# Performance work log

Hardware: AMD Instinct MI355X
Metric: run time of the kernel (lower is better)

## Reference

```python
import jax, jax.numpy as jnp
import numpy as np

B = 8        # number of clouds
NP = 4096    # points per cloud
STRIDE = 4   # sampler stride -> NS = NP // STRIDE sampled centers per cloud
K = 32       # knn neighbours
NS = NP // STRIDE


def setup_inputs() -> dict:
    key = jax.random.key(0)
    k1, k2, k3, k4 = jax.random.split(key, 4)
    N = B * NP
    x = jax.random.normal(k1, (N, 64), dtype=jnp.float32)
    pos = jax.random.normal(k2, (N, 3), dtype=jnp.float32)
    batch = jnp.repeat(jnp.arange(B, dtype=jnp.int64), NP)
    d_in = 64 + 3
    W1 = jax.random.normal(k3, (d_in, 128), dtype=jnp.float32) / np.sqrt(d_in)
    b1 = jnp.zeros((128,), dtype=jnp.float32)
    W2 = jax.random.normal(k4, (128, 256), dtype=jnp.float32) / np.sqrt(128)
    b2 = jnp.zeros((256,), dtype=jnp.float32)
    return {"x": x, "pos": pos, "batch": batch, "W1": W1, "b1": b1, "W2": W2, "b2": b2}


def reference(x, pos, batch, W1, b1, W2, b2):
    # --- sampler: stride sampling per cloud (clouds are equal-sized, contiguous) ---
    pos_b = pos.reshape(B, NP, 3)
    idx_local = jnp.arange(0, NP, STRIDE)                       # [NS]
    idx = (idx_local[None, :] + jnp.arange(B)[:, None] * NP).reshape(-1)  # global sampled idx [B*NS]
    pos_s = pos_b[:, idx_local]                                 # [B, NS, 3]

    # --- neighbour_finder: knn within each cloud (batch-respecting via per-cloud blocks) ---
    # squared distances [B, NS, NP] without materializing [B,NS,NP,3]
    d2 = ((pos_s ** 2).sum(-1)[:, :, None]
          + (pos_b ** 2).sum(-1)[:, None, :]
          - 2.0 * jnp.einsum('bsd,bnd->bsn', pos_s, pos_b))
    _, nbr = jax.lax.top_k(-d2, K)                              # [B, NS, K] local neighbour idx
    col = (nbr + (jnp.arange(B) * NP)[:, None, None]).reshape(-1)  # global neighbour idx [E]

    # --- conv: PointNetConv -> MLP(concat(x_j, pos_j - pos_i)) then max over neighbours ---
    x_j = x[col].reshape(B, NS, K, -1)                          # [B, NS, K, 64]
    rel = pos[col].reshape(B, NS, K, 3) - pos_s[:, :, None, :]  # pos_j - pos_i
    feat = jnp.concatenate([x_j, rel], axis=-1)                 # [B, NS, K, 67]
    h = jax.nn.relu(feat @ W1 + b1)                             # [B, NS, K, 128]
    h = jax.nn.relu(h @ W2 + b2)                                # [B, NS, K, 256]
    x_out = h.max(axis=2).reshape(B * NS, -1)                   # [B*NS, 256]

    pos_out = pos_s.reshape(-1, 3)
    batch_out = batch[idx]
    return x_out, pos_out, batch_out, idx
```

## Files before the change

kernel.cpp:

```cpp
#include <hip/hip_runtime.h>
#include <hip/hip_bf16.h>

#define BB 8
#define NP 4096
#define STRIDE 4
#define KNN 32
#define NS (NP/STRIDE)
#define NQ (BB*NS)
#define DIN 67
#define H1N 128
#define H2N 256

typedef __attribute__((ext_vector_type(8)))  short bf16x8;
typedef __attribute__((ext_vector_type(16))) float f32x16;
typedef __attribute__((ext_vector_type(8)))  short short8;

__device__ __forceinline__ unsigned int f2u(float f) {
    unsigned int b = __float_as_uint(f);
    return (b & 0x80000000u) ? ~b : (b | 0x80000000u);
}
__device__ __forceinline__ short f2bf(float f) {
    unsigned u = __float_as_uint(f);
    unsigned r = u + 0x7FFFu + ((u >> 16) & 1u);
    return (short)(r >> 16);
}

__global__ __launch_bounds__(256) void knn_kernel(const float* __restrict__ pos,
                                                  int* __restrict__ col) {
    __shared__ unsigned long long surv[NP];
    __shared__ unsigned int pvt[4];
    __shared__ int scount;

    const int q    = blockIdx.x;
    const int b    = q >> 10;
    const int s    = q & (NS - 1);
    const int qi   = b * NP + s * STRIDE;
    const int t    = threadIdx.x;
    const int lane = t & 63;

    if (t == 64) pvt[3] = 0xFFFFFFFFu;

    const float qx = pos[qi*3+0], qy = pos[qi*3+1], qz = pos[qi*3+2];
    const float q2 = __fadd_rn(__fadd_rn(__fmul_rn(qx,qx), __fmul_rn(qy,qy)), __fmul_rn(qz,qz));

    const float* pb = pos + (size_t)b * NP * 3;
    unsigned int myk[16];
    #pragma unroll
    for (int i = 0; i < 4; ++i) {
        const int u = t + i * 256;
        const float4* pp = (const float4*)(pb + (size_t)u * 12);
        const float4 v0 = pp[0], v1 = pp[1], v2 = pp[2];
        const float px[4] = {v0.x, v0.w, v1.z, v2.y};
        const float py[4] = {v0.y, v1.x, v1.w, v2.z};
        const float pz[4] = {v0.z, v1.y, v2.x, v2.w};
        #pragma unroll
        for (int j = 0; j < 4; ++j) {
            const float p2 = __fadd_rn(__fadd_rn(__fmul_rn(px[j],px[j]), __fmul_rn(py[j],py[j])), __fmul_rn(pz[j],pz[j]));
            const float dt = __fadd_rn(__fadd_rn(__fmul_rn(qx,px[j]), __fmul_rn(qy,py[j])), __fmul_rn(qz,pz[j]));
            const float d2 = __fsub_rn(__fadd_rn(q2, p2), __fmul_rn(2.0f, dt));
            myk[i*4+j] = f2u(d2);
        }
    }

    if (t < 64) {
        const unsigned int mk = myk[0];
        int rank = 0;
        #pragma unroll
        for (int ss = 0; ss < 64; ++ss) {
            const unsigned int ks = __shfl(mk, ss, 64);
            rank += (int)((ks < mk) | ((ks == mk) & (ss < t)));
        }
        if (rank == 1)  pvt[0] = mk;
        if (rank == 4)  pvt[1] = mk;
        if (rank == 16) pvt[2] = mk;
    }
    __syncthreads();

    int C = 0;
    for (int level = 0; level < 4 && C < KNN; ++level) {
        __syncthreads();
        if (t == 0) scount = 0;
        __syncthreads();
        const unsigned int T = pvt[level];
        #pragma unroll
        for (int i = 0; i < 16; ++i) {
            const bool p = (myk[i] <= T);
            const unsigned long long mask = __ballot(p);
            const int cnt = __popcll(mask);
            int base = 0;
            if (lane == 0 && cnt) base = atomicAdd(&scount, cnt);
            base = __shfl(base, 0, 64);
            if (p) {
                const int off = __popcll(mask & ((1ull << lane) - 1ull));
                const int n   = 4 * (t + (i >> 2) * 256) + (i & 3);
                surv[base + off] = ((unsigned long long)myk[i] << 32) | (unsigned int)n;
            }
        }
        __syncthreads();
        C = scount;
    }

    const int L = C;
    for (int j = t; j < L; j += 256) {
        const unsigned long long v = surv[j];
        int rank = 0;
        #pragma unroll 4
        for (int ss = 0; ss < L; ++ss)
            rank += (int)(surv[ss] < v);
        if (rank < KNN)
            col[q * KNN + rank] = b * NP + (int)(unsigned int)(v & 0xFFFFFFFFull);
    }
}

__global__ __launch_bounds__(64) void prep_w1(const float* __restrict__ W1,
                                              short* __restrict__ W1T) {
    const int nt = blockIdx.x / 5, t = blockIdx.x % 5;
    const int l  = threadIdx.x;
    const int c  = 32*nt + (l & 31);
    short8 v;
    #pragma unroll
    for (int b = 0; b < 8; ++b) {
        const int k = 16*t + 8*(l >> 5) + b;
        v[b] = (k < DIN) ? f2bf(W1[k * H1N + c]) : (short)0;
    }
    *(short8*)(W1T + ((size_t)(nt*5 + t) * 64 + l) * 8) = v;
}

__global__ __launch_bounds__(64) void prep_w2(const float* __restrict__ W2,
                                              short* __restrict__ W2T) {
    const int nt = blockIdx.x >> 3, t = blockIdx.x & 7;
    const int l  = threadIdx.x;
    const int c  = 32*nt + (l & 31);
    short8 v;
    #pragma unroll
    for (int b = 0; b < 8; ++b) {
        const int k = 16*t + 8*(l >> 5) + b;
        v[b] = f2bf(W2[k * H2N + c]);
    }
    *(short8*)(W2T + ((size_t)(nt*8 + t) * 64 + l) * 8) = v;
}

__global__ __launch_bounds__(256, 2) void mlp_mfma(const float* __restrict__ x,
                                                   const float* __restrict__ pos,
                                                   const int* __restrict__ col,
                                                   const float* __restrict__ b1,
                                                   const float* __restrict__ b2,
                                                   const short* __restrict__ W1T,
                                                   const short* __restrict__ W2T,
                                                   float* __restrict__ out) {
    __shared__ __align__(16) short feat[128 * 80];
    __shared__ __align__(16) short h1s [128 * 128];

    const int q0 = blockIdx.x * 4;
    const int t  = threadIdx.x;
    const int w  = t >> 6, l = t & 63;

    {
        const int row  = t >> 1, part = t & 1;
        const int q    = q0 + (row >> 5);
        const int c    = col[q * KNN + (row & 31)];
        const float4* xr = (const float4*)(x + (size_t)c * 64 + part * 32);
        short* fr = feat + row * 80 + part * 32;
        #pragma unroll
        for (int i = 0; i < 8; ++i) {
            const float4 v = xr[i];
            *(int*)(fr + i * 4 + 0) = (int)((unsigned short)f2bf(v.x) | ((unsigned)(unsigned short)f2bf(v.y) << 16));
            *(int*)(fr + i * 4 + 2) = (int)((unsigned short)f2bf(v.z) | ((unsigned)(unsigned short)f2bf(v.w) << 16));
        }
        if (part == 0) {
            const int b  = q >> 10;
            const int qi = b * NP + (q & (NS - 1)) * STRIDE;
            short8 o;
            o[0] = f2bf(pos[c*3+0] - pos[qi*3+0]);
            o[1] = f2bf(pos[c*3+1] - pos[qi*3+1]);
            o[2] = f2bf(pos[c*3+2] - pos[qi*3+2]);
            o[3] = 0; o[4] = 0; o[5] = 0; o[6] = 0; o[7] = 0;
            *(short8*)(feat + row * 80 + 64) = o;
            short8 z = {0,0,0,0,0,0,0,0};
            *(short8*)(feat + row * 80 + 72) = z;
        }
    }
    __syncthreads();

    const int lr = l & 31;
    const int lh = l >> 5;

    {
        bf16x8 w1f[20];
        #pragma unroll
        for (int i = 0; i < 20; ++i)
            w1f[i] = *(const bf16x8*)(W1T + ((size_t)i * 64 + l) * 8);

        bf16x8 a1[5];
        #pragma unroll
        for (int kt = 0; kt < 5; ++kt) {
            const int row = 32*w + lr;
            a1[kt] = *(const bf16x8*)(feat + row * 80 + 16*kt + 8*lh);
        }

        #pragma unroll
        for (int nt = 0; nt < 4; ++nt) {
            const float bv = b1[32*nt + lr];
            f32x16 acc;
            #pragma unroll
            for (int r = 0; r < 16; ++r) acc[r] = bv;
            #pragma unroll
            for (int kt = 0; kt < 5; ++kt)
                acc = __builtin_amdgcn_mfma_f32_32x32x16_bf16(a1[kt], w1f[nt*5 + kt], acc, 0, 0, 0);
            #pragma unroll
            for (int r = 0; r < 16; ++r) {
                const int i   = (r & 3) + 8*(r >> 2) + 4*lh;
                const int row = 32*w + i;
                const int c   = 32*nt + lr;
                const int adr = row * 128 + ((((c >> 3) ^ (row & 15)) << 3) | (c & 7));
                h1s[adr] = f2bf(fmaxf(acc[r], 0.0f));
            }
        }
    }
    __syncthreads();

    {
        bf16x8 a2[8];
        #pragma unroll
        for (int kt = 0; kt < 8; ++kt) {
            const int row  = 32*w + lr;
            const int slot = 2*kt + lh;
            a2[kt] = *(const bf16x8*)(h1s + row * 128 + ((slot ^ (row & 15)) << 3));
        }

        f32x16 acc[8];
        #pragma unroll
        for (int nt = 0; nt < 8; ++nt)
            #pragma unroll
            for (int r = 0; r < 16; ++r) acc[nt][r] = 0.0f;

        bf16x8 cur[8];
        #pragma unroll
        for (int kt = 0; kt < 8; ++kt)
            cur[kt] = *(const bf16x8*)(W2T + ((size_t)kt * 64 + l) * 8);

        #pragma unroll
        for (int nt = 0; nt < 8; ++nt) {
            bf16x8 nxt[8];
            if (nt < 7) {
                #pragma unroll
                for (int kt = 0; kt < 8; ++kt)
                    nxt[kt] = *(const bf16x8*)(W2T + ((size_t)((nt+1)*8 + kt) * 64 + l) * 8);
            }
            #pragma unroll
            for (int kt = 0; kt < 8; ++kt)
                acc[nt] = __builtin_amdgcn_mfma_f32_32x32x16_bf16(a2[kt], cur[kt], acc[nt], 0, 0, 0);
            #pragma unroll
            for (int kt = 0; kt < 8; ++kt) cur[kt] = nxt[kt];
        }

        const int q = q0 + w;
        #pragma unroll
        for (int nt = 0; nt < 8; ++nt) {
            float m = acc[nt][0];
            #pragma unroll
            for (int r = 1; r < 16; ++r) m = fmaxf(m, acc[nt][r]);
            m = fmaxf(m, __shfl_xor(m, 32, 64));
            m = fmaxf(m + b2[32*nt + lr], 0.0f);
            if (l < 32) out[(size_t)q * H2N + 32*nt + l] = m;
        }
    }
}

__global__ __launch_bounds__(256) void tail_kernel(const float* __restrict__ pos,
                                                   float* __restrict__ out) {
    const int qn = blockIdx.x * 256 + threadIdx.x;
    if (qn >= NQ) return;
    const int b  = qn >> 10;
    const int s  = qn & (NS - 1);
    const int qi = b * NP + s * STRIDE;

    float* pos_out   = out + (size_t)NQ * H2N;
    float* batch_out = pos_out + (size_t)NQ * 3;
    float* idx_out   = batch_out + NQ;

    pos_out[qn*3+0] = pos[qi*3+0];
    pos_out[qn*3+1] = pos[qi*3+1];
    pos_out[qn*3+2] = pos[qi*3+2];
    batch_out[qn]   = (float)b;
    idx_out[qn]     = (float)qi;
}

extern "C" void kernel_launch(void* const* d_in, const int* in_sizes, int n_in,
                              void* d_out, int out_size, void* d_ws, size_t ws_size,
                              hipStream_t stream) {
    const float* x   = (const float*)d_in[0];
    const float* pos = (const float*)d_in[1];
    const float* W1  = (const float*)d_in[3];
    const float* b1  = (const float*)d_in[4];
    const float* W2  = (const float*)d_in[5];
    const float* b2  = (const float*)d_in[6];
    float* out = (float*)d_out;

    char* ws   = (char*)d_ws;
    int*  col  = (int*)ws;
    short* W1T = (short*)(ws + 1048576);
    short* W2T = (short*)(ws + 1048576 + 20480);

    prep_w1<<<20, 64, 0, stream>>>(W1, W1T);
    prep_w2<<<64, 64, 0, stream>>>(W2, W2T);
    knn_kernel<<<NQ, 256, 0, stream>>>(pos, col);
    mlp_mfma<<<NQ/4, 256, 0, stream>>>(x, pos, col, b1, b2, W1T, W2T, out);
    tail_kernel<<<(NQ + 255) / 256, 256, 0, stream>>>(pos, out);
}
```

Measured before the change: 156.0 us.

## Count survivors per threshold before compaction and vectorize rank scan

The KNN selection now counts survivors per wave with ballots for each threshold level and compacts only once, at the first level that yields at least K candidates. Per-ballot atomics on a shared counter are replaced by deterministic per-wave prefix offsets. The pivot ranks are lowered (1/3/8 instead of 1/4/16), giving tighter thresholds and a smaller survivor set. The final rank scan reads pairs of 64-bit keys per shared-memory load. Tighter pivots may fall through to wider levels more often, which costs extra count passes.

```diff
diff --git a/kernel.cpp b/kernel.cpp
--- a/kernel.cpp
+++ b/kernel.cpp
@@ -27,15 +27,16 @@
 
 __global__ __launch_bounds__(256) void knn_kernel(const float* __restrict__ pos,
                                                   int* __restrict__ col) {
-    __shared__ unsigned long long surv[NP];
+    __shared__ __align__(16) unsigned long long surv[NP];
     __shared__ unsigned int pvt[4];
-    __shared__ int scount;
+    __shared__ int cnts[4];
 
     const int q    = blockIdx.x;
     const int b    = q >> 10;
     const int s    = q & (NS - 1);
     const int qi   = b * NP + s * STRIDE;
     const int t    = threadIdx.x;
+    const int w    = t >> 6;
     const int lane = t & 63;
 
     if (t == 64) pvt[3] = 0xFFFFFFFFu;
@@ -70,43 +71,56 @@
             const unsigned int ks = __shfl(mk, ss, 64);
             rank += (int)((ks < mk) | ((ks == mk) & (ss < t)));
         }
-        if (rank == 1)  pvt[0] = mk;
-        if (rank == 4)  pvt[1] = mk;
-        if (rank == 16) pvt[2] = mk;
+        if (rank == 1) pvt[0] = mk;
+        if (rank == 3) pvt[1] = mk;
+        if (rank == 8) pvt[2] = mk;
     }
     __syncthreads();
 
-    int C = 0;
-    for (int level = 0; level < 4 && C < KNN; ++level) {
+    int C = 0, level = 0;
+    for (; level < 4; ++level) {
+        const unsigned int T = pvt[level];
+        int cw = 0;
+        #pragma unroll
+        for (int i = 0; i < 16; ++i)
+            cw += __popcll(__ballot(myk[i] <= T));
+        if (lane == 0) cnts[w] = cw;
         __syncthreads();
-        if (t == 0) scount = 0;
+        C = cnts[0] + cnts[1] + cnts[2] + cnts[3];
+        if (C >= KNN) break;
         __syncthreads();
+    }
+
+    {
         const unsigned int T = pvt[level];
+        int base = 0;
+        #pragma unroll
+        for (int i = 0; i < 4; ++i) base += (i < w) ? cnts[i] : 0;
         #pragma unroll
         for (int i = 0; i < 16; ++i) {
             const bool p = (myk[i] <= T);
             const unsigned long long mask = __ballot(p);
-            const int cnt = __popcll(mask);
-            int base = 0;
-            if (lane == 0 && cnt) base = atomicAdd(&scount, cnt);
-            base = __shfl(base, 0, 64);
             if (p) {
                 const int off = __popcll(mask & ((1ull << lane) - 1ull));
                 const int n   = 4 * (t + (i >> 2) * 256) + (i & 3);
                 surv[base + off] = ((unsigned long long)myk[i] << 32) | (unsigned int)n;
             }
-        }
-        __syncthreads();
-        C = scount;
-    }
-
-    const int L = C;
-    for (int j = t; j < L; j += 256) {
+            base += __popcll(mask);
+        }
+    }
+    __syncthreads();
+
+    const ulonglong2* sp2 = (const ulonglong2*)surv;
+    const int C2 = C >> 1;
+    for (int j = t; j < C; j += 256) {
         const unsigned long long v = surv[j];
         int rank = 0;
         #pragma unroll 4
-        for (int ss = 0; ss < L; ++ss)
-            rank += (int)(surv[ss] < v);
+        for (int ss = 0; ss < C2; ++ss) {
+            const ulonglong2 pr = sp2[ss];
+            rank += (int)(pr.x < v) + (int)(pr.y < v);
+        }
+        if (C & 1) rank += (int)(surv[C - 1] < v);
         if (rank < KNN)
             col[q * KNN + rank] = b * NP + (int)(unsigned int)(v & 0xFFFFFFFFull);
     }
```

Measured after the change: 160.2 us. +2.7%, slower.

## Run kNN one query per wavefront and fuse tail and weight-prep kernels

Applied to the files above, without the earlier changes.

The kNN kernel now gives each query one wavefront instead of a full 256-thread block. Distances are recomputed during each threshold compaction pass, and pivots are chosen from a 64-point strided sample with an adaptive threshold retry loop. This removes the block-level barriers, the shared atomics and the register-held keys. The tail outputs are folded into the kNN kernel and the two weight-prep kernels are merged into one, which cuts launch count. In exchange, distances may be recomputed several times per query, and survivors are capped at 1024 per wave. Hitting that cap could truncate candidates.

```diff
diff --git a/kernel.cpp b/kernel.cpp
--- a/kernel.cpp
+++ b/kernel.cpp
@@ -10,6 +10,7 @@
 #define DIN 67
 #define H1N 128
 #define H2N 256
+#define SCAPW 1024
 
 typedef __attribute__((ext_vector_type(8)))  short bf16x8;
 typedef __attribute__((ext_vector_type(16))) float f32x16;
@@ -26,118 +27,139 @@
 }
 
 __global__ __launch_bounds__(256) void knn_kernel(const float* __restrict__ pos,
-                                                  int* __restrict__ col) {
-    __shared__ unsigned long long surv[NP];
-    __shared__ unsigned int pvt[4];
-    __shared__ int scount;
-
-    const int q    = blockIdx.x;
+                                                  int* __restrict__ col,
+                                                  float* __restrict__ out) {
+    __shared__ __align__(16) unsigned long long surv[4][SCAPW];
+
+    const int t    = threadIdx.x;
+    const int w    = t >> 6;
+    const int lane = t & 63;
+    const int q    = blockIdx.x * 4 + w;
     const int b    = q >> 10;
     const int s    = q & (NS - 1);
     const int qi   = b * NP + s * STRIDE;
-    const int t    = threadIdx.x;
-    const int lane = t & 63;
-
-    if (t == 64) pvt[3] = 0xFFFFFFFFu;
 
     const float qx = pos[qi*3+0], qy = pos[qi*3+1], qz = pos[qi*3+2];
     const float q2 = __fadd_rn(__fadd_rn(__fmul_rn(qx,qx), __fmul_rn(qy,qy)), __fmul_rn(qz,qz));
-
     const float* pb = pos + (size_t)b * NP * 3;
-    unsigned int myk[16];
+
+    {
+        float* pos_out   = out + (size_t)NQ * H2N;
+        float* batch_out = pos_out + (size_t)NQ * 3;
+        float* idx_out   = batch_out + NQ;
+        if (lane < 3)       pos_out[q*3+lane] = pos[qi*3+lane];
+        else if (lane == 3) batch_out[q] = (float)b;
+        else if (lane == 4) idx_out[q]   = (float)qi;
+    }
+
+    unsigned int skey;
+    {
+        const int n = lane * 64;
+        const float px = pb[n*3+0], py = pb[n*3+1], pz = pb[n*3+2];
+        const float p2 = __fadd_rn(__fadd_rn(__fmul_rn(px,px), __fmul_rn(py,py)), __fmul_rn(pz,pz));
+        const float dt = __fadd_rn(__fadd_rn(__fmul_rn(qx,px), __fmul_rn(qy,py)), __fmul_rn(qz,pz));
+        skey = f2u(__fsub_rn(__fadd_rn(q2, p2), __fmul_rn(2.0f, dt)));
+    }
+    int srk = 0;
     #pragma unroll
-    for (int i = 0; i < 4; ++i) {
-        const int u = t + i * 256;
-        const float4* pp = (const float4*)(pb + (size_t)u * 12);
-        const float4 v0 = pp[0], v1 = pp[1], v2 = pp[2];
-        const float px[4] = {v0.x, v0.w, v1.z, v2.y};
-        const float py[4] = {v0.y, v1.x, v1.w, v2.z};
-        const float pz[4] = {v0.z, v1.y, v2.x, v2.w};
-        #pragma unroll
-        for (int j = 0; j < 4; ++j) {
-            const float p2 = __fadd_rn(__fadd_rn(__fmul_rn(px[j],px[j]), __fmul_rn(py[j],py[j])), __fmul_rn(pz[j],pz[j]));
-            const float dt = __fadd_rn(__fadd_rn(__fmul_rn(qx,px[j]), __fmul_rn(qy,py[j])), __fmul_rn(qz,pz[j]));
-            const float d2 = __fsub_rn(__fadd_rn(q2, p2), __fmul_rn(2.0f, dt));
-            myk[i*4+j] = f2u(d2);
-        }
-    }
-
-    if (t < 64) {
-        const unsigned int mk = myk[0];
-        int rank = 0;
-        #pragma unroll
-        for (int ss = 0; ss < 64; ++ss) {
-            const unsigned int ks = __shfl(mk, ss, 64);
-            rank += (int)((ks < mk) | ((ks == mk) & (ss < t)));
-        }
-        if (rank == 1)  pvt[0] = mk;
-        if (rank == 4)  pvt[1] = mk;
-        if (rank == 16) pvt[2] = mk;
-    }
-    __syncthreads();
-
-    int C = 0;
-    for (int level = 0; level < 4 && C < KNN; ++level) {
-        __syncthreads();
-        if (t == 0) scount = 0;
-        __syncthreads();
-        const unsigned int T = pvt[level];
-        #pragma unroll
-        for (int i = 0; i < 16; ++i) {
-            const bool p = (myk[i] <= T);
-            const unsigned long long mask = __ballot(p);
-            const int cnt = __popcll(mask);
-            int base = 0;
-            if (lane == 0 && cnt) base = atomicAdd(&scount, cnt);
-            base = __shfl(base, 0, 64);
-            if (p) {
-                const int off = __popcll(mask & ((1ull << lane) - 1ull));
-                const int n   = 4 * (t + (i >> 2) * 256) + (i & 3);
-                surv[base + off] = ((unsigned long long)myk[i] << 32) | (unsigned int)n;
+    for (int ss = 0; ss < 64; ++ss) {
+        const unsigned int ks = (unsigned int)__shfl((int)skey, ss, 64);
+        srk += (int)((ks < skey) | ((ks == skey) & (ss < lane)));
+    }
+    unsigned int T0, T1, T2, T3, T4;
+    {
+        unsigned long long m;
+        m = __ballot(srk == 0);  T0 = (unsigned int)__shfl((int)skey, (int)__builtin_ctzll(m), 64);
+        m = __ballot(srk == 1);  T1 = (unsigned int)__shfl((int)skey, (int)__builtin_ctzll(m), 64);
+        m = __ballot(srk == 3);  T2 = (unsigned int)__shfl((int)skey, (int)__builtin_ctzll(m), 64);
+        m = __ballot(srk == 8);  T3 = (unsigned int)__shfl((int)skey, (int)__builtin_ctzll(m), 64);
+        m = __ballot(srk == 31); T4 = (unsigned int)__shfl((int)skey, (int)__builtin_ctzll(m), 64);
+    }
+
+    unsigned long long* sw = surv[w];
+
+    auto compact = [&](unsigned int T) -> int {
+        int base = 0;
+        #pragma unroll 4
+        for (int j4 = 0; j4 < 16; ++j4) {
+            const int n0 = j4 * 256 + lane * 4;
+            const float4* pp = (const float4*)(pb + (size_t)n0 * 3);
+            const float4 v0 = pp[0], v1 = pp[1], v2 = pp[2];
+            const float px[4] = {v0.x, v0.w, v1.z, v2.y};
+            const float py[4] = {v0.y, v1.x, v1.w, v2.z};
+            const float pz[4] = {v0.z, v1.y, v2.x, v2.w};
+            #pragma unroll
+            for (int jj = 0; jj < 4; ++jj) {
+                const float p2 = __fadd_rn(__fadd_rn(__fmul_rn(px[jj],px[jj]), __fmul_rn(py[jj],py[jj])), __fmul_rn(pz[jj],pz[jj]));
+                const float dt = __fadd_rn(__fadd_rn(__fmul_rn(qx,px[jj]), __fmul_rn(qy,py[jj])), __fmul_rn(qz,pz[jj]));
+                const unsigned int k = f2u(__fsub_rn(__fadd_rn(q2, p2), __fmul_rn(2.0f, dt)));
+                const bool psel = (k <= T);
+                const unsigned long long mask = __ballot(psel);
+                if (psel) {
+                    const int idx = base + (int)__popcll(mask & ((1ull << lane) - 1ull));
+                    if (idx < SCAPW)
+                        sw[idx] = ((unsigned long long)k << 32) | (unsigned int)(n0 + jj);
+                }
+                base += (int)__popcll(mask);
             }
         }
-        __syncthreads();
-        C = scount;
-    }
-
-    const int L = C;
-    for (int j = t; j < L; j += 256) {
-        const unsigned long long v = surv[j];
-        int rank = 0;
+        return base;
+    };
+
+    int lvl = 1, C = 0;
+    #pragma unroll 1
+    for (int att = 0; att < 4; ++att) {
+        const unsigned int T = (lvl == 0) ? T0 : (lvl == 1) ? T1 : (lvl == 2) ? T2 : (lvl == 3) ? T3 : T4;
+        C = compact(T);
+        if (C >= KNN && C <= SCAPW) break;
+        if (C < KNN) { if (lvl >= 4) break; ++lvl; }
+        else         { if (lvl == 0) break; lvl = 0; }
+    }
+    if (C > SCAPW) C = SCAPW;
+
+    const ulonglong2* sp2 = (const ulonglong2*)sw;
+    const int C2 = C >> 1;
+    for (int j = lane; j < C; j += 64) {
+        const unsigned long long v = sw[j];
+        int rk = 0;
         #pragma unroll 4
-        for (int ss = 0; ss < L; ++ss)
-            rank += (int)(surv[ss] < v);
-        if (rank < KNN)
-            col[q * KNN + rank] = b * NP + (int)(unsigned int)(v & 0xFFFFFFFFull);
-    }
-}
-
-__global__ __launch_bounds__(64) void prep_w1(const float* __restrict__ W1,
-                                              short* __restrict__ W1T) {
-    const int nt = blockIdx.x / 5, t = blockIdx.x % 5;
-    const int l  = threadIdx.x;
-    const int c  = 32*nt + (l & 31);
-    short8 v;
-    #pragma unroll
-    for (int b = 0; b < 8; ++b) {
-        const int k = 16*t + 8*(l >> 5) + b;
-        v[b] = (k < DIN) ? f2bf(W1[k * H1N + c]) : (short)0;
-    }
-    *(short8*)(W1T + ((size_t)(nt*5 + t) * 64 + l) * 8) = v;
-}
-
-__global__ __launch_bounds__(64) void prep_w2(const float* __restrict__ W2,
-                                              short* __restrict__ W2T) {
-    const int nt = blockIdx.x >> 3, t = blockIdx.x & 7;
-    const int l  = threadIdx.x;
-    const int c  = 32*nt + (l & 31);
-    short8 v;
-    #pragma unroll
-    for (int b = 0; b < 8; ++b) {
-        const int k = 16*t + 8*(l >> 5) + b;
-        v[b] = f2bf(W2[k * H2N + c]);
-    }
-    *(short8*)(W2T + ((size_t)(nt*8 + t) * 64 + l) * 8) = v;
+        for (int ss = 0; ss < C2; ++ss) {
+            const ulonglong2 pr = sp2[ss];
+            rk += (int)(pr.x < v) + (int)(pr.y < v);
+        }
+        if (C & 1) rk += (int)(sw[C - 1] < v);
+        if (rk < KNN)
+            col[q * KNN + rk] = b * NP + (int)(unsigned int)(v & 0xFFFFFFFFull);
+    }
+}
+
+__global__ __launch_bounds__(64) void prep_w(const float* __restrict__ W1,
+                                             const float* __restrict__ W2,
+                                             short* __restrict__ W1T,
+                                             short* __restrict__ W2T) {
+    const int l = threadIdx.x;
+    if (blockIdx.x < 20) {
+        const int nt = blockIdx.x / 5, t = blockIdx.x % 5;
+        const int c  = 32*nt + (l & 31);
+        short8 v;
+        #pragma unroll
+        for (int b = 0; b < 8; ++b) {
+            const int k = 16*t + 8*(l >> 5) + b;
+            v[b] = (k < DIN) ? f2bf(W1[k * H1N + c]) : (short)0;
+        }
+        *(short8*)(W1T + ((size_t)(nt*5 + t) * 64 + l) * 8) = v;
+    } else {
+        const int bb = blockIdx.x - 20;
+        const int nt = bb >> 3, t = bb & 7;
+        const int c  = 32*nt + (l & 31);
+        short8 v;
+        #pragma unroll
+        for (int b = 0; b < 8; ++b) {
+            const int k = 16*t + 8*(l >> 5) + b;
+            v[b] = f2bf(W2[k * H2N + c]);
+        }
+        *(short8*)(W2T + ((size_t)(nt*8 + t) * 64 + l) * 8) = v;
+    }
 }
 
 __global__ __launch_bounds__(256, 2) void mlp_mfma(const float* __restrict__ x,
@@ -267,25 +289,6 @@
     }
 }
 
-__global__ __launch_bounds__(256) void tail_kernel(const float* __restrict__ pos,
-                                                   float* __restrict__ out) {
-    const int qn = blockIdx.x * 256 + threadIdx.x;
-    if (qn >= NQ) return;
-    const int b  = qn >> 10;
-    const int s  = qn & (NS - 1);
-    const int qi = b * NP + s * STRIDE;
-
-    float* pos_out   = out + (size_t)NQ * H2N;
-    float* batch_out = pos_out + (size_t)NQ * 3;
-    float* idx_out   = batch_out + NQ;
-
-    pos_out[qn*3+0] = pos[qi*3+0];
-    pos_out[qn*3+1] = pos[qi*3+1];
-    pos_out[qn*3+2] = pos[qi*3+2];
-    batch_out[qn]   = (float)b;
-    idx_out[qn]     = (float)qi;
-}
-
 extern "C" void kernel_launch(void* const* d_in, const int* in_sizes, int n_in,
                               void* d_out, int out_size, void* d_ws, size_t ws_size,
                               hipStream_t stream) {
@@ -302,9 +305,7 @@
     short* W1T = (short*)(ws + 1048576);
     short* W2T = (short*)(ws + 1048576 + 20480);
 
-    prep_w1<<<20, 64, 0, stream>>>(W1, W1T);
-    prep_w2<<<64, 64, 0, stream>>>(W2, W2T);
-    knn_kernel<<<NQ, 256, 0, stream>>>(pos, col);
+    prep_w<<<84, 64, 0, stream>>>(W1, W2, W1T, W2T);
+    knn_kernel<<<NQ/4, 256, 0, stream>>>(pos, col, out);
     mlp_mfma<<<NQ/4, 256, 0, stream>>>(x, pos, col, b1, b2, W1T, W2T, out);
-    tail_kernel<<<(NQ + 255) / 256, 256, 0, stream>>>(pos, out);
-}
+}
```

New measurement: 206.4 us. 32.4% more time.
